# Performance work log

Measured on AMD Instinct MI355X. Metric: run time of the kernel, lower is better.

## Reference

```python
import jax, jax.numpy as jnp
import numpy as np

B, C, H = 64, 64, 32

def _pm_cross_pairs(ks):
    # Replicates PM_cross(2, ks): pairs (i, i+j) ordered by gap j=1..ks-1, then i.
    a, b = [], []
    for j in range(1, ks):
        for i in range(ks - j):
            a.append(i)
            b.append(i + j)
    return np.array(a, dtype=np.int32), np.array(b, dtype=np.int32)

def setup_inputs() -> dict:
    key = jax.random.key(0)
    k1, k2 = jax.random.split(key)
    ia, ib = _pm_cross_pairs(H)           # 496 pairs for H=32
    hk = ia.shape[0] + 2 * H              # 560
    x = jax.random.normal(k1, (B, C, H, H), dtype=jnp.float32)
    weight = 0.1 * jax.random.normal(k2, (C, H, hk, H), dtype=jnp.float32)
    return {"x": x, "weight": weight, "idx_a": jnp.asarray(ia), "idx_b": jnp.asarray(ib)}

def reference(x, weight, idx_a, idx_b):
    # cross-term products along last axis: [B,C,H,P]
    cross = x[..., idx_a] * x[..., idx_b]
    feat = jnp.concatenate([x, x * x, cross], axis=-1)  # [B,C,H,Hk]
    # per-(channel,row) grouped matmul
    return jnp.einsum('bcij,cijo->bcio', feat, weight)
```

## Files before the change

kernel.cpp:

```cpp
#include <hip/hip_runtime.h>

#define NB 64
#define NC 64
#define NH 32
#define HK 560
#define XSTR 57

typedef __bf16 bf16x8 __attribute__((ext_vector_type(8)));
typedef float f32x4 __attribute__((ext_vector_type(4)));

__global__ __launch_bounds__(256, 4) void hconv_kernel(
    const float* __restrict__ x, const float* __restrict__ w,
    const int* __restrict__ idx_a, const int* __restrict__ idx_b,
    float* __restrict__ out)
{
    __shared__ __align__(16) float smem[4 * 64 * 33];
    float* s_x = smem;
    unsigned short* s_wtu = (unsigned short*)&smem[NB * XSTR];

    const int t = threadIdx.x;
    const int g = blockIdx.x;
    const int c = g >> 5, i = g & 31;

    const int wv = t >> 6, lane = t & 63;
    const int lr = lane & 15, lq = lane >> 4;
    const float* wbase = w + (size_t)(c * NH + i) * HK * NH;
    const int xrow = t >> 2, seg = t & 3;
    const float* xr = x + (((size_t)xrow * NC + c) * NH + i) * NH + seg * 8;

    float4 v0 = *(const float4*)(xr);
    float4 v1 = *(const float4*)(xr + 4);

#define BLK(J) ((unsigned)(64 + ((J) - 1) * 32 - ((J) * ((J) - 1)) / 2))
    unsigned d6[6];
    #pragma unroll
    for (int st = 0; st < 6; ++st) {
        unsigned pa, pb, ko;
        if (st < 4) {
            pa = 8u + 8u * (unsigned)lq;
            if (lq <= 1) {
                const int j = wv * 4 + st + 1;
                pb = pa + (unsigned)j; ko = BLK(j) + 8u * (unsigned)lq;
            } else if (lq == 2) {
                if (wv == 3 && st == 3) { pb = 24u; ko = 48u; }
                else { const int j = wv * 4 + st + 1;
                       pb = 24u + (unsigned)j; ko = BLK(j) + 16u; }
            } else {
                if (wv == 0) { const int j = st + 1; pb = 32u + (unsigned)j; ko = BLK(j) + 24u; }
                else if (wv == 1) {
                    if (st < 3) { const int j = st + 5; pb = 32u + (unsigned)j; ko = BLK(j) + 24u; }
                    else        { pb = 32u; ko = 56u; }
                } else if (wv == 2) {
                    if (st == 0) { pb = 48u; ko = 24u; }
                    else         { pb = 48u; ko = 1023u; }
                } else               { pb = 48u; ko = 1023u; }
            }
        } else if (st == 4) {
            if (wv == 0)      { const int j = 17 + lq; pa = 8u;  pb = 8u + (unsigned)j;  ko = BLK(j); }
            else if (wv == 1) { const int j = 22 + lq; pa = 8u;  pb = 8u + (unsigned)j;  ko = BLK(j); }
            else if (wv == 2) {
                if (lq == 0)      { pa = 8u; pb = 36u; ko = 550u; }
                else if (lq == 1) { pa = 6u; pb = 35u; ko = 552u; }
                else if (lq == 2) { pa = 3u; pb = 33u; ko = 552u; }
                else              { pa = 1u; pb = 32u; ko = 552u; }
            } else            { const int j = 17 + lq; pa = 16u; pb = 16u + (unsigned)j; ko = BLK(j) + 8u; }
        } else {
            if (wv == 0) {
                if (lq == 0) { pa = 8u; pb = 29u; ko = BLK(21); }
                else         { pa = 0u; pb = 0u;  ko = 1023u; }
            } else if (wv == 1) {
                if (lq == 0)      { pa = 8u; pb = 34u; ko = BLK(26); }
                else if (lq == 1) { pa = 8u; pb = 35u; ko = BLK(27); }
                else              { pa = 0u; pb = 0u;  ko = 1023u; }
            } else if (wv == 2) {
                if (lq == 0)      { pa = 8u;  pb = 8u;  ko = 32u; }
                else if (lq == 1) { pa = 8u;  pb = 48u; ko = 0u;  }
                else if (lq == 2) { pa = 16u; pb = 16u; ko = 40u; }
                else              { pa = 16u; pb = 48u; ko = 8u;  }
            } else {
                if (lq == 0)      { pa = 16u; pb = 37u; ko = BLK(21) + 8u; }
                else if (lq == 1) { pa = 16u; pb = 38u; ko = BLK(22) + 8u; }
                else if (lq == 2) { pa = 16u; pb = 39u; ko = BLK(23) + 8u; }
                else              { pa = 24u; pb = 48u; ko = 16u; }
            }
        }
        d6[st] = pa | (pb << 6) | (ko << 12);
    }
#undef BLK

    f32x4 gA[4], gB[4];

#define GLOAD(G, K) { \
    _Pragma("unroll") \
    for (int o_ = 0; o_ < 4; ++o_) { \
        unsigned dd_ = (unsigned)__builtin_amdgcn_readlane((int)d6[K], 16 * o_); \
        unsigned ko_ = (dd_ >> 12) & 1023u; \
        if (ko_ != 1023u) { \
            const float* wp_ = wbase + (size_t)ko_ * NH + 4 * lane; \
            G[o_] = *(const f32x4*)wp_; \
        } else { \
            G[o_] = (f32x4){0.f, 0.f, 0.f, 0.f}; \
        } } }

    GLOAD(gA, 0);
    GLOAD(gB, 1);

    {
        float* dst = &s_x[xrow * XSTR + 8 + seg * 8];
        dst[0] = v0.x; dst[1] = v0.y; dst[2] = v0.z; dst[3] = v0.w;
        dst[4] = v1.x; dst[5] = v1.y; dst[6] = v1.z; dst[7] = v1.w;
        if (seg == 0) {
            float* r0 = &s_x[xrow * XSTR];
            #pragma unroll
            for (int m = 0; m < 8; ++m) {
                r0[m] = 0.0f;
                r0[40 + m] = 0.0f;
                r0[48 + m] = 1.0f;
            }
        }
    }

    f32x4 acc[4][2];
    #pragma unroll
    for (int r = 0; r < 4; ++r) {
        acc[r][0] = (f32x4){0.f, 0.f, 0.f, 0.f};
        acc[r][1] = (f32x4){0.f, 0.f, 0.f, 0.f};
    }

#define SWRITE(G) { \
    unsigned short* tb_ = s_wtu + wv * 1088 + (lane >> 3) * 34 + (lane & 7) * 4; \
    _Pragma("unroll") \
    for (int o_ = 0; o_ < 4; ++o_) \
        _Pragma("unroll") \
        for (int w_ = 0; w_ < 4; ++w_) \
            tb_[o_ * 272 + w_] = \
                __builtin_bit_cast(unsigned short, (__bf16)G[o_][w_]); \
    asm volatile("" ::: "memory"); }

    __syncthreads();

    float qx[4][8];
    #pragma unroll
    for (int rt = 0; rt < 4; ++rt)
        #pragma unroll
        for (int m = 0; m < 8; ++m)
            qx[rt][m] = s_x[(rt * 16 + lr) * XSTR + 8 + 8 * lq + m];

#define STEP(ST, GEN, DOLD, GLD, DOWR, GWR) { \
    bf16x8 b0_, b1_; \
    { const unsigned short* rb_ = s_wtu + (wv * 4 + lq) * 272 + lr; \
      _Pragma("unroll") \
      for (int j_ = 0; j_ < 8; ++j_) { \
          b0_[j_] = __builtin_bit_cast(__bf16, rb_[j_ * 34]); \
          b1_[j_] = __builtin_bit_cast(__bf16, rb_[j_ * 34 + 16]); } } \
    if (DOLD) GLOAD(GLD, (ST) + 2); \
    if (DOWR) SWRITE(GWR); \
    const unsigned d_ = d6[ST]; \
    const int paf_ = (int)(d_ & 63u), pbf_ = (int)((d_ >> 6) & 63u); \
    _Pragma("unroll") \
    for (int rt_ = 0; rt_ < 4; ++rt_) { \
        const float* xr_ = &s_x[(rt_ * 16 + lr) * XSTR]; \
        const float* qb_ = xr_ + pbf_; \
        bf16x8 a_; \
        if (GEN) { \
            const float* qa_ = xr_ + paf_; \
            _Pragma("unroll") \
            for (int j_ = 0; j_ < 8; ++j_) a_[j_] = (__bf16)(qa_[j_] * qb_[j_]); \
        } else { \
            _Pragma("unroll") \
            for (int j_ = 0; j_ < 8; ++j_) a_[j_] = (__bf16)(qx[rt_][j_] * qb_[j_]); \
        } \
        acc[rt_][0] = __builtin_amdgcn_mfma_f32_16x16x32_bf16(a_, b0_, acc[rt_][0], 0, 0, 0); \
        acc[rt_][1] = __builtin_amdgcn_mfma_f32_16x16x32_bf16(a_, b1_, acc[rt_][1], 0, 0, 0); } }

    SWRITE(gA);
    STEP(0, 0, 1, gA, 1, gB);
    STEP(1, 0, 1, gB, 1, gA);
    STEP(2, 0, 1, gA, 1, gB);
    STEP(3, 0, 1, gB, 1, gA);
    STEP(4, 1, 0, gA, 1, gB);
    STEP(5, 1, 0, gA, 0, gA);

#undef STEP
#undef SWRITE
#undef GLOAD

    __syncthreads();

    #pragma unroll
    for (int rt = 0; rt < 4; ++rt)
        #pragma unroll
        for (int nh = 0; nh < 2; ++nh)
            #pragma unroll
            for (int r = 0; r < 4; ++r)
                smem[(wv * NB + rt * 16 + lq * 4 + r) * 33 + nh * 16 + lr] =
                    acc[rt][nh][r];

    __syncthreads();

    {
        const int b = t >> 2, m0 = (t & 3) * 8;
        float s0[8];
        #pragma unroll
        for (int m = 0; m < 8; ++m) s0[m] = smem[b * 33 + m0 + m];
        #pragma unroll
        for (int wv2 = 1; wv2 < 4; ++wv2)
            #pragma unroll
            for (int m = 0; m < 8; ++m)
                s0[m] += smem[(wv2 * NB + b) * 33 + m0 + m];
        float* op = out + (((size_t)b * NC + c) * NH + i) * NH + m0;
        float4 o0 = {s0[0], s0[1], s0[2], s0[3]};
        float4 o1 = {s0[4], s0[5], s0[6], s0[7]};
        *(float4*)op = o0;
        *(float4*)(op + 4) = o1;
    }
}

extern "C" void kernel_launch(void* const* d_in, const int* in_sizes, int n_in,
                              void* d_out, int out_size, void* d_ws, size_t ws_size,
                              hipStream_t stream) {
    const float* x = (const float*)d_in[0];
    const float* w = (const float*)d_in[1];
    const int* idx_a = (const int*)d_in[2];
    const int* idx_b = (const int*)d_in[3];
    float* out = (float*)d_out;
    hconv_kernel<<<dim3(NC * NH), dim3(256), 0, stream>>>(x, w, idx_a, idx_b, out);
}
```

Baseline: 236.8 us.

## Process two (channel,row) tiles per block with cross-tile weight prefetch

Each block now handles two consecutive rows i for the same channel, halving the grid. Both x rows are staged in shared memory up front, and the first weight stages of the second tile are prefetched during the tail of the first, so the pipeline does not restart. The epilogue reduction is restructured to a two-buffer accumulate to fit the larger shared footprint. In exchange, fewer blocks run (1024 instead of 2048), shared memory use grows, and more barriers are added.

```diff
diff --git a/kernel.cpp b/kernel.cpp
--- a/kernel.cpp
+++ b/kernel.cpp
@@ -14,22 +14,28 @@
     const int* __restrict__ idx_a, const int* __restrict__ idx_b,
     float* __restrict__ out)
 {
-    __shared__ __align__(16) float smem[4 * 64 * 33];
-    float* s_x = smem;
-    unsigned short* s_wtu = (unsigned short*)&smem[NB * XSTR];
+    __shared__ __align__(16) float smem[9472];
+    float* s_x0 = smem;
+    float* s_x1 = smem + 3648;
+    unsigned short* s_wtu = (unsigned short*)(smem + 7296);
+    float* red0 = smem;
+    float* red1 = smem + 7296;
 
     const int t = threadIdx.x;
     const int g = blockIdx.x;
-    const int c = g >> 5, i = g & 31;
+    const int c = g >> 4, ip = (g & 15) << 1;
 
     const int wv = t >> 6, lane = t & 63;
     const int lr = lane & 15, lq = lane >> 4;
-    const float* wbase = w + (size_t)(c * NH + i) * HK * NH;
+    const float* wb0 = w + (size_t)(c * NH + ip) * HK * NH;
+    const float* wb1 = wb0 + (size_t)HK * NH;
     const int xrow = t >> 2, seg = t & 3;
-    const float* xr = x + (((size_t)xrow * NC + c) * NH + i) * NH + seg * 8;
-
-    float4 v0 = *(const float4*)(xr);
-    float4 v1 = *(const float4*)(xr + 4);
+    const float* xg = x + (((size_t)xrow * NC + c) * NH + ip) * NH + seg * 16;
+
+    float4 v0 = *(const float4*)(xg);
+    float4 v1 = *(const float4*)(xg + 4);
+    float4 v2 = *(const float4*)(xg + 8);
+    float4 v3 = *(const float4*)(xg + 12);
 
 #define BLK(J) ((unsigned)(64 + ((J) - 1) * 32 - ((J) * ((J) - 1)) / 2))
     unsigned d6[6];
@@ -90,27 +96,30 @@
 
     f32x4 gA[4], gB[4];
 
-#define GLOAD(G, K) { \
+#define GLOAD(G, WB, K) { \
     _Pragma("unroll") \
     for (int o_ = 0; o_ < 4; ++o_) { \
         unsigned dd_ = (unsigned)__builtin_amdgcn_readlane((int)d6[K], 16 * o_); \
         unsigned ko_ = (dd_ >> 12) & 1023u; \
         if (ko_ != 1023u) { \
-            const float* wp_ = wbase + (size_t)ko_ * NH + 4 * lane; \
+            const float* wp_ = (WB) + (size_t)ko_ * NH + 4 * lane; \
             G[o_] = *(const f32x4*)wp_; \
         } else { \
             G[o_] = (f32x4){0.f, 0.f, 0.f, 0.f}; \
         } } }
 
-    GLOAD(gA, 0);
-    GLOAD(gB, 1);
+    GLOAD(gA, wb0, 0);
+    GLOAD(gB, wb0, 1);
 
     {
-        float* dst = &s_x[xrow * XSTR + 8 + seg * 8];
-        dst[0] = v0.x; dst[1] = v0.y; dst[2] = v0.z; dst[3] = v0.w;
-        dst[4] = v1.x; dst[5] = v1.y; dst[6] = v1.z; dst[7] = v1.w;
-        if (seg == 0) {
-            float* r0 = &s_x[xrow * XSTR];
+        float* plane = s_x0 + (seg >> 1) * 3648;
+        float* dst = plane + xrow * XSTR + 8 + (seg & 1) * 16;
+        dst[0] = v0.x; dst[1] = v0.y; dst[2]  = v0.z; dst[3]  = v0.w;
+        dst[4] = v1.x; dst[5] = v1.y; dst[6]  = v1.z; dst[7]  = v1.w;
+        dst[8] = v2.x; dst[9] = v2.y; dst[10] = v2.z; dst[11] = v2.w;
+        dst[12] = v3.x; dst[13] = v3.y; dst[14] = v3.z; dst[15] = v3.w;
+        if ((seg & 1) == 0) {
+            float* r0 = plane + xrow * XSTR;
             #pragma unroll
             for (int m = 0; m < 8; ++m) {
                 r0[m] = 0.0f;
@@ -137,29 +146,29 @@
                 __builtin_bit_cast(unsigned short, (__bf16)G[o_][w_]); \
     asm volatile("" ::: "memory"); }
 
-    __syncthreads();
+#define QXFILL(SXP) { \
+    _Pragma("unroll") \
+    for (int rt_ = 0; rt_ < 4; ++rt_) \
+        _Pragma("unroll") \
+        for (int m_ = 0; m_ < 8; ++m_) \
+            qx[rt_][m_] = (SXP)[(rt_ * 16 + lr) * XSTR + 8 + 8 * lq + m_]; }
 
     float qx[4][8];
-    #pragma unroll
-    for (int rt = 0; rt < 4; ++rt)
-        #pragma unroll
-        for (int m = 0; m < 8; ++m)
-            qx[rt][m] = s_x[(rt * 16 + lr) * XSTR + 8 + 8 * lq + m];
-
-#define STEP(ST, GEN, DOLD, GLD, DOWR, GWR) { \
+
+#define STEP(SXP, ST, GEN, DOLD, GLD, GLB, GLK, DOWR, GWR) { \
     bf16x8 b0_, b1_; \
     { const unsigned short* rb_ = s_wtu + (wv * 4 + lq) * 272 + lr; \
       _Pragma("unroll") \
       for (int j_ = 0; j_ < 8; ++j_) { \
           b0_[j_] = __builtin_bit_cast(__bf16, rb_[j_ * 34]); \
           b1_[j_] = __builtin_bit_cast(__bf16, rb_[j_ * 34 + 16]); } } \
-    if (DOLD) GLOAD(GLD, (ST) + 2); \
+    if (DOLD) GLOAD(GLD, GLB, GLK); \
     if (DOWR) SWRITE(GWR); \
     const unsigned d_ = d6[ST]; \
     const int paf_ = (int)(d_ & 63u), pbf_ = (int)((d_ >> 6) & 63u); \
     _Pragma("unroll") \
     for (int rt_ = 0; rt_ < 4; ++rt_) { \
-        const float* xr_ = &s_x[(rt_ * 16 + lr) * XSTR]; \
+        const float* xr_ = &(SXP)[(rt_ * 16 + lr) * XSTR]; \
         const float* qb_ = xr_ + pbf_; \
         bf16x8 a_; \
         if (GEN) { \
@@ -173,47 +182,79 @@
         acc[rt_][0] = __builtin_amdgcn_mfma_f32_16x16x32_bf16(a_, b0_, acc[rt_][0], 0, 0, 0); \
         acc[rt_][1] = __builtin_amdgcn_mfma_f32_16x16x32_bf16(a_, b1_, acc[rt_][1], 0, 0, 0); } }
 
+#define EPILOG(IOUT, TRAIL) { \
+    __syncthreads(); \
+    if (wv < 2) { \
+        float* bw_ = (wv == 0) ? red0 : red1; \
+        _Pragma("unroll") \
+        for (int rt_ = 0; rt_ < 4; ++rt_) \
+            _Pragma("unroll") \
+            for (int nh_ = 0; nh_ < 2; ++nh_) \
+                _Pragma("unroll") \
+                for (int r_ = 0; r_ < 4; ++r_) \
+                    bw_[(rt_ * 16 + lq * 4 + r_) * 33 + nh_ * 16 + lr] = acc[rt_][nh_][r_]; \
+    } \
+    __syncthreads(); \
+    if (wv >= 2) { \
+        float* bw_ = (wv == 2) ? red0 : red1; \
+        _Pragma("unroll") \
+        for (int rt_ = 0; rt_ < 4; ++rt_) \
+            _Pragma("unroll") \
+            for (int nh_ = 0; nh_ < 2; ++nh_) \
+                _Pragma("unroll") \
+                for (int r_ = 0; r_ < 4; ++r_) { \
+                    const int ix_ = (rt_ * 16 + lq * 4 + r_) * 33 + nh_ * 16 + lr; \
+                    bw_[ix_] += acc[rt_][nh_][r_]; } \
+    } \
+    __syncthreads(); \
+    { \
+        const int b_ = t >> 2, m0_ = (t & 3) * 8; \
+        float s0_[8]; \
+        _Pragma("unroll") \
+        for (int m_ = 0; m_ < 8; ++m_) \
+            s0_[m_] = red0[b_ * 33 + m0_ + m_] + red1[b_ * 33 + m0_ + m_]; \
+        float* op_ = out + (((size_t)b_ * NC + c) * NH + ip + (IOUT)) * NH + m0_; \
+        float4 o0_ = {s0_[0], s0_[1], s0_[2], s0_[3]}; \
+        float4 o1_ = {s0_[4], s0_[5], s0_[6], s0_[7]}; \
+        *(float4*)op_ = o0_; \
+        *(float4*)(op_ + 4) = o1_; \
+    } \
+    if (TRAIL) __syncthreads(); }
+
+    __syncthreads();
+
+    QXFILL(s_x0);
     SWRITE(gA);
-    STEP(0, 0, 1, gA, 1, gB);
-    STEP(1, 0, 1, gB, 1, gA);
-    STEP(2, 0, 1, gA, 1, gB);
-    STEP(3, 0, 1, gB, 1, gA);
-    STEP(4, 1, 0, gA, 1, gB);
-    STEP(5, 1, 0, gA, 0, gA);
+    STEP(s_x0, 0, 0, 1, gA, wb0, 2, 1, gB);
+    STEP(s_x0, 1, 0, 1, gB, wb0, 3, 1, gA);
+    STEP(s_x0, 2, 0, 1, gA, wb0, 4, 1, gB);
+    STEP(s_x0, 3, 0, 1, gB, wb0, 5, 1, gA);
+    STEP(s_x0, 4, 1, 1, gA, wb1, 0, 1, gB);
+    STEP(s_x0, 5, 1, 1, gB, wb1, 1, 0, gA);
+
+    QXFILL(s_x1);
+    EPILOG(0, 1);
+
+    #pragma unroll
+    for (int r = 0; r < 4; ++r) {
+        acc[r][0] = (f32x4){0.f, 0.f, 0.f, 0.f};
+        acc[r][1] = (f32x4){0.f, 0.f, 0.f, 0.f};
+    }
+    SWRITE(gA);
+    STEP(s_x1, 0, 0, 1, gA, wb1, 2, 1, gB);
+    STEP(s_x1, 1, 0, 1, gB, wb1, 3, 1, gA);
+    STEP(s_x1, 2, 0, 1, gA, wb1, 4, 1, gB);
+    STEP(s_x1, 3, 0, 1, gB, wb1, 5, 1, gA);
+    STEP(s_x1, 4, 1, 0, gA, wb1, 0, 1, gB);
+    STEP(s_x1, 5, 1, 0, gA, wb1, 0, 0, gA);
+
+    EPILOG(1, 0);
 
 #undef STEP
+#undef QXFILL
 #undef SWRITE
 #undef GLOAD
-
-    __syncthreads();
-
-    #pragma unroll
-    for (int rt = 0; rt < 4; ++rt)
-        #pragma unroll
-        for (int nh = 0; nh < 2; ++nh)
-            #pragma unroll
-            for (int r = 0; r < 4; ++r)
-                smem[(wv * NB + rt * 16 + lq * 4 + r) * 33 + nh * 16 + lr] =
-                    acc[rt][nh][r];
-
-    __syncthreads();
-
-    {
-        const int b = t >> 2, m0 = (t & 3) * 8;
-        float s0[8];
-        #pragma unroll
-        for (int m = 0; m < 8; ++m) s0[m] = smem[b * 33 + m0 + m];
-        #pragma unroll
-        for (int wv2 = 1; wv2 < 4; ++wv2)
-            #pragma unroll
-            for (int m = 0; m < 8; ++m)
-                s0[m] += smem[(wv2 * NB + b) * 33 + m0 + m];
-        float* op = out + (((size_t)b * NC + c) * NH + i) * NH + m0;
-        float4 o0 = {s0[0], s0[1], s0[2], s0[3]};
-        float4 o1 = {s0[4], s0[5], s0[6], s0[7]};
-        *(float4*)op = o0;
-        *(float4*)(op + 4) = o1;
-    }
+#undef EPILOG
 }
 
 extern "C" void kernel_launch(void* const* d_in, const int* in_sizes, int n_in,
@@ -224,5 +265,5 @@
     const int* idx_a = (const int*)d_in[2];
     const int* idx_b = (const int*)d_in[3];
     float* out = (float*)d_out;
-    hconv_kernel<<<dim3(NC * NH), dim3(256), 0, stream>>>(x, w, idx_a, idx_b, out);
+    hconv_kernel<<<dim3(NC * NH / 2), dim3(256), 0, stream>>>(x, w, idx_a, idx_b, out);
 }
```

Result: no change. 239.6 us (+1.2%).
